# Kernel tuning notes

Hardware: AMD Instinct MI355X
Metric: run time of the kernel (lower is better)

Reference implementation:

```python
import jax, jax.numpy as jnp
import numpy as np

SIGMA = 10
POPULATIONS = 2
LR = 0.001


def _normalize(L, prior):
    # clamp then normalize over populations (logsumexp across the population axis)
    O = L.shape[1]
    L = jnp.clip(L, -5.0, 0.0)
    lse = jax.nn.logsumexp(L.reshape(POPULATIONS, -1, O), axis=0)  # (in/P, O)
    L = L - jnp.tile(lse, (POPULATIONS, 1))
    prior = jnp.clip(prior, -5.0, 0.0)
    prior = prior - jax.nn.logsumexp(prior)
    return L, prior


def _forward(x, L, prior):
    B, T, IN = x.shape
    O = L.shape[1]
    L, prior = _normalize(L, prior)  # matches normalize_probs() in __init__

    # membrane potential: OR of spikes over trailing window of SIGMA steps
    xb = x.astype(bool)
    pot = xb
    for s in range(1, SIGMA):  # fixed small loop (sigma=10)
        pot = pot | jnp.pad(xb, ((0, 0), (s, 0), (0, 0)))[:, :T, :]

    tpre0 = jnp.full((B, IN), -T, dtype=jnp.int32)
    tpost0 = jnp.full((B, O), jnp.iinfo(jnp.int32).max, dtype=jnp.int32)
    base_key = jax.random.key(42)

    pot_T = jnp.transpose(pot, (1, 0, 2))  # (T,B,IN)
    x_T = jnp.transpose(xb, (1, 0, 2))

    def step(carry, inp):
        L, prior, tpre, tpost, t = carry
        pot_t, x_t = inp
        potf = pot_t.astype(L.dtype)
        logits = potf @ L + prior  # (B,O), logits <= 0 so exp is safe
        # torch: softmax(exp(logits)).multinomial == categorical with logits=exp(logits)
        key = jax.random.fold_in(base_key, t)
        widx = jax.random.categorical(key, jnp.exp(logits), axis=-1)  # (B,)
        win = jax.nn.one_hot(widx, O, dtype=L.dtype)
        # trace updates happen BEFORE STDP, as in the torch code
        tpre = jnp.where(x_t, 0, tpre - 1)
        tpost = jnp.where(win > 0, 0, tpost - 1)
        ltp = (tpre >= -SIGMA).astype(L.dtype)
        ltd = (tpre < -SIGMA).astype(L.dtype)
        post = (tpost < 0).astype(L.dtype)
        m_ltp = jnp.einsum('bi,bo->io', ltp, win) / B
        m_ltd = jnp.einsum('bi,bo->io', ltd, win) / B
        m_pp = jnp.einsum('bi,bo->io', potf, post) / B
        decay = (t + 1).astype(L.dtype)  # lr_decay_inverse starts at 1
        # dw = (5 e^{-L} - 1) * LTP.mean - LTD.mean - pre_post.mean ; LTD was negated
        dw = (5.0 * jnp.exp(-L) - 1.0) * m_ltp + m_ltd - m_pp
        L2 = L + (LR / decay) * dw
        wm = jnp.mean(win, axis=0)
        db = (-5.0 * prior - 1.0) * wm - (1.0 - wm)
        p2 = prior + (LR / decay) * db
        L2, p2 = _normalize(L2, p2)
        return (L2, p2, tpre, tpost, t + 1), None

    (Lf, pf, _, _, _), _ = jax.lax.scan(
        step, (L, prior, tpre0, tpost0, jnp.int32(0)), (pot_T, x_T))
    return jnp.concatenate([Lf.reshape(-1), pf])


def setup_inputs() -> dict:
    key = jax.random.key(0)
    k1, k2, k3 = jax.random.split(key, 3)
    B, T, IN, O = 256, 200, 1568, 100
    x = jax.random.randint(k1, (B, T, IN), 0, 2, dtype=jnp.int32)
    log_likelihood = jax.random.uniform(k2, (IN, O), dtype=jnp.float32) * -1.0 - 1.0
    log_prior = jax.random.uniform(k3, (O,), dtype=jnp.float32) * -1.0 - 1.0
    return {"x": x, "log_likelihood": log_likelihood, "log_prior": log_prior}


def reference(x, log_likelihood, log_prior):
    return _forward(x, log_likelihood, log_prior)
```

## Files before the change

kernel.cpp:

```cpp
#include <hip/hip_runtime.h>
#include <stdint.h>

#define BB 256
#define TT 200
#define INN 1568
#define OO 100
#define PAIRS 784
#define NHALF 12800

typedef unsigned long long u64;
typedef __attribute__((ext_vector_type(4))) int v4i;

typedef const __attribute__((address_space(1))) uint32_t* gas_p;
typedef __attribute__((address_space(3))) uint32_t* las_p;
#define GLD16(g, l) __builtin_amdgcn_global_load_lds((gas_p)(g), (las_p)(l), 16, 0, 0)

__device__ __forceinline__ void tf_round(uint32_t& x0, uint32_t& x1, int r) {
    x0 += x1;
    x1 = (x1 << r) | (x1 >> (32 - r));
    x1 ^= x0;
}

__device__ __forceinline__ void threefry(uint32_t k0, uint32_t k1,
                                         uint32_t x0, uint32_t x1,
                                         uint32_t& o0, uint32_t& o1) {
    uint32_t k2 = k0 ^ k1 ^ 0x1BD11BDAu;
    x0 += k0; x1 += k1;
    tf_round(x0,x1,13); tf_round(x0,x1,15); tf_round(x0,x1,26); tf_round(x0,x1,6);
    x0 += k1; x1 += k2 + 1u;
    tf_round(x0,x1,17); tf_round(x0,x1,29); tf_round(x0,x1,16); tf_round(x0,x1,24);
    x0 += k2; x1 += k0 + 2u;
    tf_round(x0,x1,13); tf_round(x0,x1,15); tf_round(x0,x1,26); tf_round(x0,x1,6);
    x0 += k0; x1 += k1 + 3u;
    tf_round(x0,x1,17); tf_round(x0,x1,29); tf_round(x0,x1,16); tf_round(x0,x1,24);
    x0 += k1; x1 += k2 + 4u;
    tf_round(x0,x1,13); tf_round(x0,x1,15); tf_round(x0,x1,26); tf_round(x0,x1,6);
    o0 = x0 + k2; o1 = x1 + k0 + 5u;
}

__global__ __launch_bounds__(256) void k_winbit(const int* __restrict__ x,
                                                uint8_t* __restrict__ widx,
                                                u64* __restrict__ bitB) {
    int tid = threadIdx.x;
    if (blockIdx.x < 200) {
        int idx = blockIdx.x * 256 + tid;
        int t = idx >> 8, b = idx & 255;
        uint32_t fk0, fk1;
        threefry(0u, 42u, 0u, (uint32_t)t, fk0, fk1);
        uint32_t bestkey = 0u;
        int bo = 0;
        int nbase = b * OO;
        for (int o = 0; o < OO; ++o) {
            uint32_t n = (uint32_t)(nbase + o);
            uint32_t lo = (n < NHALF) ? n : n - NHALF;
            uint32_t v0, v1;
            threefry(fk0, fk1, lo, lo + NHALF, v0, v1);
            uint32_t bits = (n < NHALF) ? v0 : v1;
            uint32_t key = bits >> 9;
            if (key > bestkey) { bestkey = key; bo = o; }
        }
        widx[idx] = (uint8_t)bo;
        return;
    }
    int pb = blockIdx.x - 200;
    int wb = pb / 100;
    int t0 = (pb - wb * 100) * 2;
    const v4i* xp = (const v4i*)x;
    u64 acc[4][4];
    #pragma unroll
    for (int q = 0; q < 4; ++q)
        #pragma unroll
        for (int c = 0; c < 4; ++c) acc[q][c] = 0;
    bool x4 = (tid < 16);
    for (int bl = 0; bl < 64; ++bl) {
        size_t base = ((size_t)((wb * 64 + bl) * TT + t0)) * 392;
        u64 bit = 1ull << bl;
        #pragma unroll
        for (int q = 0; q < 3; ++q) {
            v4i v = __builtin_nontemporal_load(&xp[base + tid + q * 256]);
            if (v.x) acc[q][0] |= bit;
            if (v.y) acc[q][1] |= bit;
            if (v.z) acc[q][2] |= bit;
            if (v.w) acc[q][3] |= bit;
        }
        if (x4) {
            v4i v = __builtin_nontemporal_load(&xp[base + tid + 768]);
            if (v.x) acc[3][0] |= bit;
            if (v.y) acc[3][1] |= bit;
            if (v.z) acc[3][2] |= bit;
            if (v.w) acc[3][3] |= bit;
        }
    }
    #pragma unroll
    for (int q = 0; q < 4; ++q) {
        if (q == 3 && !x4) continue;
        int p = tid + q * 256;
        int tp = (p >= 392) ? 1 : 0;
        int iq = p - tp * 392;
        u64* dst = bitB + ((size_t)((t0 + tp) * 4 + wb)) * INN + iq * 4;
        dst[0] = acc[q][0]; dst[1] = acc[q][1];
        dst[2] = acc[q][2]; dst[3] = acc[q][3];
    }
}

__global__ __launch_bounds__(256) void k_fwpost(const uint8_t* __restrict__ widx,
                                                u64* __restrict__ winbits,
                                                u64* __restrict__ postbits,
                                                uint32_t* __restrict__ cnt) {
    __shared__ uint32_t wl32[TT * 65];
    __shared__ int fwl[BB];
    int o = blockIdx.x;
    int tid = threadIdx.x;
    const uint32_t* wsrc = (const uint32_t*)widx;
    for (int g = tid; g < TT * 64; g += 256) {
        int t = g >> 6, w = g & 63;
        wl32[t * 65 + w] = wsrc[g];
    }
    __syncthreads();
    if (tid < 64) {
        int f0 = 255, f1 = 255, f2 = 255, f3 = 255;
        for (int t = 0; t < TT; ++t) {
            uint32_t w4 = wl32[t * 65 + tid];
            if (((w4      ) & 255u) == (uint32_t)o && f0 == 255) f0 = t;
            if (((w4 >>  8) & 255u) == (uint32_t)o && f1 == 255) f1 = t;
            if (((w4 >> 16) & 255u) == (uint32_t)o && f2 == 255) f2 = t;
            if (((w4 >> 24) & 255u) == (uint32_t)o && f3 == 255) f3 = t;
        }
        fwl[4 * tid + 0] = f0; fwl[4 * tid + 1] = f1;
        fwl[4 * tid + 2] = f2; fwl[4 * tid + 3] = f3;
    }
    __syncthreads();
    if (tid < TT) {
        int t = tid;
        u64 wbA[4], pbA[4];
        uint32_t c = 0;
        #pragma unroll
        for (int k = 0; k < 4; ++k) {
            u64 wacc = 0, pacc = 0;
            for (int q2 = 0; q2 < 16; ++q2) {
                uint32_t w4 = wl32[t * 65 + k * 16 + q2];
                #pragma unroll
                for (int j = 0; j < 4; ++j) {
                    int bl = q2 * 4 + j;
                    bool win = (((w4 >> (8 * j)) & 255u) == (uint32_t)o);
                    c += win ? 1u : 0u;
                    bool post = (fwl[k * 64 + q2 * 4 + j] < t) && !win;
                    u64 bit = 1ull << bl;
                    if (win)  wacc |= bit;
                    if (post) pacc |= bit;
                }
            }
            wbA[k] = wacc; pbA[k] = pacc;
        }
        size_t base = (size_t)(t * OO + o) * 4;
        #pragma unroll
        for (int k = 0; k < 4; ++k) {
            winbits[base + k] = wbA[k];
            postbits[base + k] = pbA[k];
        }
        cnt[t * OO + o] = c;
    }
}

#define PBLK 16
#define OBLK 20
#define FTHR 320
#define ROWSTRIDE (4 * INN)
#define PFD 6
#define RS 16

__global__ __launch_bounds__(FTHR) void k_fused(
        const float* __restrict__ L0,
        const float* __restrict__ p0arr,
        const u64* __restrict__ bitB,
        const u64* __restrict__ winbits,
        const u64* __restrict__ postbits,
        const uint32_t* __restrict__ cnt,
        float* __restrict__ outL,
        float* __restrict__ outp) {
    if (blockIdx.x == 49) {
        if (blockIdx.y != 0) return;
        int l = threadIdx.x;
        if (l >= 64) return;
        bool has2 = (l + 64) < OO;
        float pa = p0arr[l];
        float pb = has2 ? p0arr[l + 64] : -1e30f;
        auto normalize = [&]() {
            pa = fminf(fmaxf(pa, -5.0f), 0.0f);
            if (has2) pb = fminf(fmaxf(pb, -5.0f), 0.0f);
            float mx = has2 ? fmaxf(pa, pb) : pa;
            #pragma unroll
            for (int s = 32; s > 0; s >>= 1) mx = fmaxf(mx, __shfl_xor(mx, s, 64));
            float sm = expf(pa - mx) + (has2 ? expf(pb - mx) : 0.0f);
            #pragma unroll
            for (int s = 32; s > 0; s >>= 1) sm += __shfl_xor(sm, s, 64);
            float lse = logf(sm) + mx;
            pa -= lse;
            if (has2) pb -= lse;
        };
        normalize();
        for (int t = 0; t < TT; ++t) {
            float eta = 0.001f / (float)(t + 1);
            float wma = (float)cnt[t * OO + l] * (1.0f / 256.0f);
            pa += eta * ((-5.0f * pa - 1.0f) * wma - (1.0f - wma));
            if (has2) {
                float wmb = (float)cnt[t * OO + l + 64] * (1.0f / 256.0f);
                pb += eta * ((-5.0f * pb - 1.0f) * wmb - (1.0f - wmb));
            }
            normalize();
        }
        outp[l] = pa;
        if (has2) outp[l + 64] = pb;
        return;
    }

    __shared__ __align__(16) u64 rowRing[RS][128];
    __shared__ __align__(16) u64 winRing[RS][80];
    __shared__ __align__(16) u64 postRing[RS][80];
    __shared__ __align__(16) uint32_t cntRing[RS][20];
    __shared__ __align__(16) u64 potL[2][16][10];
    __shared__ __align__(16) u64 ltpL[2][16][10];

    int tid = threadIdx.x;
    int wave = tid >> 6;
    int lane = tid & 63;
    int p0 = blockIdx.x * PBLK;
    int o0 = blockIdx.y * OBLK;

    int pl = tid & 15;
    int ol = tid >> 4;
    int o  = o0 + ol;
    int i0 = p0 + pl;
    int i1 = i0 + PAIRS;

    int lk  = lane >> 3;
    int lpq = (lane & 7) * 2;
    const u64* rowsrc = bitB + (size_t)((lk & 3) * INN + (lk >> 2) * PAIRS + p0 + lpq);

    int wpl = tid & 15;
    int wk  = tid >> 4;
    int eidx = wk * 16 + wpl;

    auto issue = [&](int s) {
        int rr = (s < TT) ? s : (TT - 1);
        int slot = s & (RS - 1);
        if (wave == 0) {
            GLD16(rowsrc + (size_t)rr * ROWSTRIDE, &rowRing[slot][2 * lane]);
        } else if (wave == 1) {
            if (lane < 40)
                GLD16(winbits + ((size_t)rr * OO + o0) * 4 + 2 * lane,
                      &winRing[slot][2 * lane]);
        } else if (wave == 2) {
            if (lane < 40)
                GLD16(postbits + ((size_t)rr * OO + o0) * 4 + 2 * lane,
                      &postRing[slot][2 * lane]);
        } else if (wave == 3) {
            if (lane < 5)
                GLD16(cnt + ((size_t)rr * OO + o0) + 4 * lane,
                      &cntRing[slot][4 * lane]);
        }
    };

    for (int s = 0; s < PFD; ++s) issue(s);
    if (wave < 4) asm volatile("s_waitcnt vmcnt(0)" ::: "memory");
    __builtin_amdgcn_s_barrier();
    if (tid < 128) {
        u64 r0 = rowRing[0][eidx];
        potL[0][wpl][wk] = r0;
        ltpL[0][wpl][wk] = r0;
    }
    float a  = L0[(size_t)i0 * OO + o];
    float b2 = L0[(size_t)i1 * OO + o];
    a  = fminf(fmaxf(a,  -5.0f), 0.0f);
    b2 = fminf(fmaxf(b2, -5.0f), 0.0f);
    {
        float m = fmaxf(a, b2), mn = fminf(a, b2);
        float lse = __logf(1.0f + __expf(mn - m)) + m;
        a -= lse; b2 -= lse;
    }
    asm volatile("s_waitcnt lgkmcnt(0)" ::: "memory");
    __builtin_amdgcn_s_barrier();

    for (int t = 0; t < TT; ++t) {
        int cur = t & 1, nxt = cur ^ 1;
        issue(t + PFD);
        int st = t & (RS - 1);
        u64 W0 = winRing[st][ol * 4 + 0], W1 = winRing[st][ol * 4 + 1];
        u64 W2 = winRing[st][ol * 4 + 2], W3 = winRing[st][ol * 4 + 3];
        u64 S0 = postRing[st][ol * 4 + 0], S1 = postRing[st][ol * 4 + 1];
        u64 S2 = postRing[st][ol * 4 + 2], S3 = postRing[st][ol * 4 + 3];
        const u64* Pp = potL[cur][pl];
        const u64* Lp = ltpL[cur][pl];
        uint32_t lt0 = __popcll(Lp[0] & W0) + __popcll(Lp[1] & W1)
                     + __popcll(Lp[2] & W2) + __popcll(Lp[3] & W3);
        uint32_t lt1 = __popcll(Lp[4] & W0) + __popcll(Lp[5] & W1)
                     + __popcll(Lp[6] & W2) + __popcll(Lp[7] & W3);
        uint32_t pp0 = __popcll(Pp[0] & S0) + __popcll(Pp[1] & S1)
                     + __popcll(Pp[2] & S2) + __popcll(Pp[3] & S3);
        uint32_t pp1 = __popcll(Pp[4] & S0) + __popcll(Pp[5] & S1)
                     + __popcll(Pp[6] & S2) + __popcll(Pp[7] & S3);
        float cwin = (float)cntRing[st][ol];
        float lt0f = (float)lt0, lt1f = (float)lt1;
        float pp0f = (float)pp0, pp1f = (float)pp1;
        float eta = 0.001f / (float)(t + 1);
        float dw0 = (5.0f * __expf(-a)  - 1.0f) * (lt0f * (1.0f/256.0f))
                  + (cwin - lt0f - pp0f) * (1.0f/256.0f);
        float dw1 = (5.0f * __expf(-b2) - 1.0f) * (lt1f * (1.0f/256.0f))
                  + (cwin - lt1f - pp1f) * (1.0f/256.0f);
        a  += eta * dw0;
        b2 += eta * dw1;
        a  = fminf(fmaxf(a,  -5.0f), 0.0f);
        b2 = fminf(fmaxf(b2, -5.0f), 0.0f);
        float m = fmaxf(a, b2), mn = fminf(a, b2);
        float lse = __logf(1.0f + __expf(mn - m)) + m;
        a -= lse; b2 -= lse;
        if (tid < 128) {
            int rbase = t + 1 - 10;
            u64 acc = 0;
            #pragma unroll
            for (int j = 1; j <= 10; ++j) {
                int rr = rbase + j; if (rr < 0) rr = 0;
                acc |= rowRing[rr & (RS - 1)][eidx];
            }
            int rz = (rbase < 0) ? 0 : rbase;
            u64 lt = acc | rowRing[rz & (RS - 1)][eidx];
            potL[nxt][wpl][wk] = acc;
            ltpL[nxt][wpl][wk] = lt;
        }
        if (wave < 4) {
            asm volatile("s_waitcnt vmcnt(4) lgkmcnt(0)" ::: "memory");
        } else {
            asm volatile("s_waitcnt lgkmcnt(0)" ::: "memory");
        }
        __builtin_amdgcn_s_barrier();
    }
    outL[(size_t)i0 * OO + o] = a;
    outL[(size_t)i1 * OO + o] = b2;
}

extern "C" void kernel_launch(void* const* d_in, const int* in_sizes, int n_in,
                              void* d_out, int out_size, void* d_ws, size_t ws_size,
                              hipStream_t stream) {
    const int*   x  = (const int*)d_in[0];
    const float* L0 = (const float*)d_in[1];
    const float* p0 = (const float*)d_in[2];
    float* out = (float*)d_out;

    char* ws = (char*)d_ws;
    size_t off = 0;
    auto alloc = [&](size_t bytes) -> void* {
        off = (off + 255) & ~(size_t)255;
        void* p = ws + off;
        off += bytes;
        return p;
    };
    uint8_t*  widx     = (uint8_t*) alloc((size_t)TT * BB);
    uint32_t* cnt      = (uint32_t*)alloc((size_t)TT * OO * 4);
    u64*      winbits  = (u64*)     alloc((size_t)TT * OO * 4 * 8);
    u64*      postbits = (u64*)     alloc((size_t)TT * OO * 4 * 8);
    u64*      bitB     = (u64*)     alloc((size_t)TT * 4 * INN * 8);
    (void)ws_size;

    hipLaunchKernelGGL(k_winbit, dim3(600), dim3(256), 0, stream, x, widx, bitB);
    hipLaunchKernelGGL(k_fwpost, dim3(OO), dim3(256), 0, stream,
                       widx, winbits, postbits, cnt);
    hipLaunchKernelGGL(k_fused, dim3(50, 5), dim3(FTHR), 0, stream,
                       L0, p0, bitB, winbits, postbits, cnt,
                       out, out + (size_t)INN * OO);
}
```

Measured before the change: 611.6 us.

## Merge three kernels into one persistent kernel with software grid barriers

```diff
diff --git a/kernel.cpp b/kernel.cpp
--- a/kernel.cpp
+++ b/kernel.cpp
@@ -7,6 +7,9 @@
 #define OO 100
 #define PAIRS 784
 #define NHALF 12800
+#define NBLK 240
+#define UNITS 686
+#define ROWSTRIDE (4 * INN)
 
 typedef unsigned long long u64;
 typedef __attribute__((ext_vector_type(4))) int v4i;
@@ -38,12 +41,47 @@
     o0 = x0 + k2; o1 = x1 + k0 + 5u;
 }
 
-__global__ __launch_bounds__(256) void k_winbit(const int* __restrict__ x,
-                                                uint8_t* __restrict__ widx,
-                                                u64* __restrict__ bitB) {
-    int tid = threadIdx.x;
-    if (blockIdx.x < 200) {
-        int idx = blockIdx.x * 256 + tid;
+struct FusedSM {
+    u64 rows[8][16][64];
+    u64 wp[8][8][128];
+    u64 potC[8][2][8][10];
+    u64 ltpC[8][2][8][10];
+    uint32_t cntR[8][8][16];
+};
+struct FwSM { uint32_t wl32[TT * 65]; int fwl[BB]; };
+union SMem { FusedSM f; FwSM w; uint32_t claim; };
+
+__device__ __forceinline__ void gridsync(uint32_t* c) {
+    __syncthreads();
+    if (threadIdx.x == 0) {
+        __threadfence();
+        __hip_atomic_fetch_add(c, 1u, __ATOMIC_ACQ_REL, __HIP_MEMORY_SCOPE_AGENT);
+        while (__hip_atomic_load(c, __ATOMIC_ACQUIRE, __HIP_MEMORY_SCOPE_AGENT)
+               < (uint32_t)NBLK)
+            __builtin_amdgcn_s_sleep(8);
+        __threadfence();
+    }
+    __syncthreads();
+}
+
+__global__ __launch_bounds__(512) void k_mono(
+        const int* __restrict__ x,
+        const float* __restrict__ L0,
+        const float* __restrict__ p0arr,
+        uint32_t* __restrict__ syncc,
+        uint8_t* __restrict__ widx,
+        uint32_t* __restrict__ cntg,
+        u64* __restrict__ winbits,
+        u64* __restrict__ postbits,
+        u64* __restrict__ bitB,
+        float* __restrict__ outL,
+        float* __restrict__ outp) {
+    __shared__ SMem sm;
+    const int tid = threadIdx.x;
+    const int bid = blockIdx.x;
+
+    if (bid < 100) {
+        int idx = bid * 512 + tid;
         int t = idx >> 8, b = idx & 255;
         uint32_t fk0, fk1;
         threefry(0u, 42u, 0u, (uint32_t)t, fk0, fk1);
@@ -60,282 +98,303 @@
             if (key > bestkey) { bestkey = key; bo = o; }
         }
         widx[idx] = (uint8_t)bo;
-        return;
     }
-    int pb = blockIdx.x - 200;
-    int wb = pb / 100;
-    int t0 = (pb - wb * 100) * 2;
-    const v4i* xp = (const v4i*)x;
-    u64 acc[4][4];
-    #pragma unroll
-    for (int q = 0; q < 4; ++q)
-        #pragma unroll
-        for (int c = 0; c < 4; ++c) acc[q][c] = 0;
-    bool x4 = (tid < 16);
-    for (int bl = 0; bl < 64; ++bl) {
-        size_t base = ((size_t)((wb * 64 + bl) * TT + t0)) * 392;
-        u64 bit = 1ull << bl;
-        #pragma unroll
-        for (int q = 0; q < 3; ++q) {
-            v4i v = __builtin_nontemporal_load(&xp[base + tid + q * 256]);
-            if (v.x) acc[q][0] |= bit;
-            if (v.y) acc[q][1] |= bit;
-            if (v.z) acc[q][2] |= bit;
-            if (v.w) acc[q][3] |= bit;
-        }
-        if (x4) {
-            v4i v = __builtin_nontemporal_load(&xp[base + tid + 768]);
-            if (v.x) acc[3][0] |= bit;
-            if (v.y) acc[3][1] |= bit;
-            if (v.z) acc[3][2] |= bit;
-            if (v.w) acc[3][3] |= bit;
-        }
+    gridsync(&syncc[0]);
+
+    if (bid < 100) {
+        const uint32_t* wsrc = (const uint32_t*)widx;
+        for (int g = tid; g < TT * 64; g += 512)
+            sm.w.wl32[(g >> 6) * 65 + (g & 63)] = wsrc[g];
+        __syncthreads();
+        int o = bid;
+        if (tid < 64) {
+            int f0 = 255, f1 = 255, f2 = 255, f3 = 255;
+            for (int t = 0; t < TT; ++t) {
+                uint32_t w4 = sm.w.wl32[t * 65 + tid];
+                if (((w4      ) & 255u) == (uint32_t)o && f0 == 255) f0 = t;
+                if (((w4 >>  8) & 255u) == (uint32_t)o && f1 == 255) f1 = t;
+                if (((w4 >> 16) & 255u) == (uint32_t)o && f2 == 255) f2 = t;
+                if (((w4 >> 24) & 255u) == (uint32_t)o && f3 == 255) f3 = t;
+            }
+            sm.w.fwl[4 * tid + 0] = f0; sm.w.fwl[4 * tid + 1] = f1;
+            sm.w.fwl[4 * tid + 2] = f2; sm.w.fwl[4 * tid + 3] = f3;
+        }
+        __syncthreads();
+        if (tid < TT) {
+            int t = tid;
+            u64 wbA[4], pbA[4];
+            uint32_t c = 0;
+            #pragma unroll
+            for (int k = 0; k < 4; ++k) {
+                u64 wacc = 0, pacc = 0;
+                for (int q2 = 0; q2 < 16; ++q2) {
+                    uint32_t w4 = sm.w.wl32[t * 65 + k * 16 + q2];
+                    #pragma unroll
+                    for (int j = 0; j < 4; ++j) {
+                        int bl = q2 * 4 + j;
+                        bool win = (((w4 >> (8 * j)) & 255u) == (uint32_t)o);
+                        c += win ? 1u : 0u;
+                        bool post = (sm.w.fwl[k * 64 + q2 * 4 + j] < t) && !win;
+                        u64 bit = 1ull << bl;
+                        if (win)  wacc |= bit;
+                        if (post) pacc |= bit;
+                    }
+                }
+                wbA[k] = wacc; pbA[k] = pacc;
+            }
+            size_t base = (size_t)(t * OO + o) * 4;
+            #pragma unroll
+            for (int k = 0; k < 4; ++k) {
+                winbits[base + k] = wbA[k];
+                postbits[base + k] = pbA[k];
+            }
+            cntg[t * OO + o] = c;
+        }
+        __syncthreads();
     }
-    #pragma unroll
-    for (int q = 0; q < 4; ++q) {
-        if (q == 3 && !x4) continue;
-        int p = tid + q * 256;
-        int tp = (p >= 392) ? 1 : 0;
-        int iq = p - tp * 392;
-        u64* dst = bitB + ((size_t)((t0 + tp) * 4 + wb)) * INN + iq * 4;
-        dst[0] = acc[q][0]; dst[1] = acc[q][1];
-        dst[2] = acc[q][2]; dst[3] = acc[q][3];
+
+    {
+        const v4i* xp = (const v4i*)x;
+        for (;;) {
+            __syncthreads();
+            if (tid == 0)
+                sm.claim = __hip_atomic_fetch_add(&syncc[2], 1u, __ATOMIC_RELAXED,
+                                                  __HIP_MEMORY_SCOPE_AGENT);
+            __syncthreads();
+            uint32_t u = sm.claim;
+            if (u >= 200u) break;
+            int wb = u & 3, tc = u >> 2;
+            u64 acc[4][4];
+            #pragma unroll
+            for (int q = 0; q < 4; ++q)
+                #pragma unroll
+                for (int c = 0; c < 4; ++c) acc[q][c] = 0;
+            bool x4 = (tid < 32);
+            for (int bl = 0; bl < 64; ++bl) {
+                size_t base = ((size_t)((wb * 64 + bl) * TT + tc * 4)) * 392;
+                u64 bit = 1ull << bl;
+                #pragma unroll
+                for (int q = 0; q < 3; ++q) {
+                    v4i v = __builtin_nontemporal_load(&xp[base + tid + q * 512]);
+                    if (v.x) acc[q][0] |= bit;
+                    if (v.y) acc[q][1] |= bit;
+                    if (v.z) acc[q][2] |= bit;
+                    if (v.w) acc[q][3] |= bit;
+                }
+                if (x4) {
+                    v4i v = __builtin_nontemporal_load(&xp[base + tid + 1536]);
+                    if (v.x) acc[3][0] |= bit;
+                    if (v.y) acc[3][1] |= bit;
+                    if (v.z) acc[3][2] |= bit;
+                    if (v.w) acc[3][3] |= bit;
+                }
+            }
+            #pragma unroll
+            for (int q = 0; q < 4; ++q) {
+                if (q == 3 && !x4) continue;
+                int p = tid + q * 512;
+                int tp = (p >= 1176) ? 3 : (p >= 784) ? 2 : (p >= 392) ? 1 : 0;
+                int iq = p - tp * 392;
+                u64* dst = bitB + ((size_t)((tc * 4 + tp) * 4 + wb)) * INN + iq * 4;
+                dst[0] = acc[q][0]; dst[1] = acc[q][1];
+                dst[2] = acc[q][2]; dst[3] = acc[q][3];
+            }
+        }
     }
-}
-
-__global__ __launch_bounds__(256) void k_fwpost(const uint8_t* __restrict__ widx,
-                                                u64* __restrict__ winbits,
-                                                u64* __restrict__ postbits,
-                                                uint32_t* __restrict__ cnt) {
-    __shared__ uint32_t wl32[TT * 65];
-    __shared__ int fwl[BB];
-    int o = blockIdx.x;
-    int tid = threadIdx.x;
-    const uint32_t* wsrc = (const uint32_t*)widx;
-    for (int g = tid; g < TT * 64; g += 256) {
-        int t = g >> 6, w = g & 63;
-        wl32[t * 65 + w] = wsrc[g];
+    gridsync(&syncc[1]);
+
+    {
+        const int wv = tid >> 6, lane = tid & 63;
+        int u = bid + NBLK * wv;
+        if (u > UNITS) return;
+        if (u == UNITS) {
+            int l = lane;
+            bool has2 = (l + 64) < OO;
+            float pa = p0arr[l];
+            float pb = has2 ? p0arr[l + 64] : -1e30f;
+            auto norm = [&]() {
+                pa = fminf(fmaxf(pa, -5.0f), 0.0f);
+                if (has2) pb = fminf(fmaxf(pb, -5.0f), 0.0f);
+                float mx = has2 ? fmaxf(pa, pb) : pa;
+                #pragma unroll
+                for (int s = 32; s > 0; s >>= 1) mx = fmaxf(mx, __shfl_xor(mx, s, 64));
+                float smv = expf(pa - mx) + (has2 ? expf(pb - mx) : 0.0f);
+                #pragma unroll
+                for (int s = 32; s > 0; s >>= 1) smv += __shfl_xor(smv, s, 64);
+                float lse = logf(smv) + mx;
+                pa -= lse;
+                if (has2) pb -= lse;
+            };
+            norm();
+            uint32_t na = cntg[l];
+            uint32_t nb = has2 ? cntg[l + 64] : 0u;
+            for (int t = 0; t < TT; ++t) {
+                float ca = (float)na, cb = (float)nb;
+                if (t < TT - 1) {
+                    na = cntg[(t + 1) * OO + l];
+                    nb = has2 ? cntg[(t + 1) * OO + l + 64] : 0u;
+                }
+                float eta = 0.001f / (float)(t + 1);
+                float wma = ca * (1.0f / 256.0f);
+                pa += eta * ((-5.0f * pa - 1.0f) * wma - (1.0f - wma));
+                if (has2) {
+                    float wmb = cb * (1.0f / 256.0f);
+                    pb += eta * ((-5.0f * pb - 1.0f) * wmb - (1.0f - wmb));
+                }
+                norm();
+            }
+            outp[l] = pa;
+            if (has2) outp[l + 64] = pb;
+            return;
+        }
+
+        const int pg = u % 98, og = u / 98;
+        const int p0 = pg * 8, o0 = og * 16;
+        const int pl = lane & 7, ol = lane >> 3;
+        const int oA = o0 + ol, oB = oA + 8;
+        const int i0 = p0 + pl, i1 = i0 + PAIRS;
+        const bool actA = (oA < OO), actB = (oB < OO);
+
+        const int e0 = (lane & 31) * 2;
+        const int wk0 = e0 >> 3, wpl0 = e0 & 7;
+        const u64* rowg = bitB + (size_t)((wk0 & 3) * INN + (wk0 >> 2) * PAIRS
+                                          + p0 + wpl0);
+        const int lw = lane & 31;
+        const u64* wpg = (lane < 32) ? winbits : postbits;
+        const bool wpact = (o0 + (lw >> 1)) < OO;
+        const bool cntact = (lane < 8) && ((o0 + (lane & 3) * 4) < OO);
+
+        auto issueG = [&](int G) {
+            int r0 = 2 * G;
+            {
+                int rr = r0 + (lane >> 5); if (rr > TT - 1) rr = TT - 1;
+                GLD16(rowg + (size_t)rr * ROWSTRIDE,
+                      (las_p)&sm.f.rows[wv][r0 & 15][0]);
+            }
+            {
+                int rr = r0; if (rr > TT - 1) rr = TT - 1;
+                if (wpact)
+                    GLD16(wpg + ((size_t)rr * OO + o0) * 4 + 2 * lw,
+                          (las_p)&sm.f.wp[wv][r0 & 7][0]);
+            }
+            {
+                int rr = r0 + 1; if (rr > TT - 1) rr = TT - 1;
+                if (wpact)
+                    GLD16(wpg + ((size_t)rr * OO + o0) * 4 + 2 * lw,
+                          (las_p)&sm.f.wp[wv][(r0 + 1) & 7][0]);
+            }
+            {
+                if (cntact) {
+                    int rr = r0 + (lane >> 2); if (rr > TT - 1) rr = TT - 1;
+                    GLD16(cntg + (size_t)rr * OO + o0 + (lane & 3) * 4,
+                          (las_p)&sm.f.cntR[wv][r0 & 7][0]);
+                }
+            }
+        };
+
+        float aA = actA ? L0[(size_t)i0 * OO + oA] : -1.0f;
+        float bA = actA ? L0[(size_t)i1 * OO + oA] : -1.0f;
+        float aB = actB ? L0[(size_t)i0 * OO + oB] : -1.0f;
+        float bB = actB ? L0[(size_t)i1 * OO + oB] : -1.0f;
+        {
+            aA = fminf(fmaxf(aA, -5.0f), 0.0f);
+            bA = fminf(fmaxf(bA, -5.0f), 0.0f);
+            float m = fmaxf(aA, bA), mn = fminf(aA, bA);
+            float lse = __logf(1.0f + __expf(mn - m)) + m;
+            aA -= lse; bA -= lse;
+            aB = fminf(fmaxf(aB, -5.0f), 0.0f);
+            bB = fminf(fmaxf(bB, -5.0f), 0.0f);
+            float m2 = fmaxf(aB, bB), mn2 = fminf(aB, bB);
+            float lse2 = __logf(1.0f + __expf(mn2 - m2)) + m2;
+            aB -= lse2; bB -= lse2;
+        }
+
+        auto chainstep = [&](int t, int sp) {
+            int s = t & 7;
+            const u64* wpS = &sm.f.wp[wv][s][0];
+            const u64* P = sm.f.potC[wv][sp][pl];
+            const u64* Lt = sm.f.ltpC[wv][sp][pl];
+            u64 P0 = P[0], P1 = P[1], P2 = P[2], P3 = P[3];
+            u64 P4 = P[4], P5 = P[5], P6 = P[6], P7 = P[7];
+            u64 Q0 = Lt[0], Q1 = Lt[1], Q2 = Lt[2], Q3 = Lt[3];
+            u64 Q4 = Lt[4], Q5 = Lt[5], Q6 = Lt[6], Q7 = Lt[7];
+            float eta = 0.001f / (float)(t + 1);
+            {
+                u64 W0 = wpS[ol*4+0], W1 = wpS[ol*4+1], W2 = wpS[ol*4+2], W3 = wpS[ol*4+3];
+                u64 S0 = wpS[64+ol*4+0], S1 = wpS[64+ol*4+1], S2 = wpS[64+ol*4+2], S3 = wpS[64+ol*4+3];
+                float cw = (float)sm.f.cntR[wv][s][ol];
+                float lt0 = (float)(__popcll(Q0&W0)+__popcll(Q1&W1)+__popcll(Q2&W2)+__popcll(Q3&W3));
+                float lt1 = (float)(__popcll(Q4&W0)+__popcll(Q5&W1)+__popcll(Q6&W2)+__popcll(Q7&W3));
+                float pp0 = (float)(__popcll(P0&S0)+__popcll(P1&S1)+__popcll(P2&S2)+__popcll(P3&S3));
+                float pp1 = (float)(__popcll(P4&S0)+__popcll(P5&S1)+__popcll(P6&S2)+__popcll(P7&S3));
+                float dw0 = (5.0f*__expf(-aA) - 1.0f)*(lt0*(1.0f/256.0f))
+                          + (cw - lt0 - pp0)*(1.0f/256.0f);
+                float dw1 = (5.0f*__expf(-bA) - 1.0f)*(lt1*(1.0f/256.0f))
+                          + (cw - lt1 - pp1)*(1.0f/256.0f);
+                aA += eta*dw0; bA += eta*dw1;
+                aA = fminf(fmaxf(aA,-5.0f),0.0f);
+                bA = fminf(fmaxf(bA,-5.0f),0.0f);
+                float m = fmaxf(aA,bA), mn = fminf(aA,bA);
+                float lse = __logf(1.0f + __expf(mn-m)) + m;
+                aA -= lse; bA -= lse;
+            }
+            {
+                u64 W0 = wpS[(ol+8)*4+0], W1 = wpS[(ol+8)*4+1], W2 = wpS[(ol+8)*4+2], W3 = wpS[(ol+8)*4+3];
+                u64 S0 = wpS[64+(ol+8)*4+0], S1 = wpS[64+(ol+8)*4+1], S2 = wpS[64+(ol+8)*4+2], S3 = wpS[64+(ol+8)*4+3];
+                float cw = (float)sm.f.cntR[wv][s][ol+8];
+                float lt0 = (float)(__popcll(Q0&W0)+__popcll(Q1&W1)+__popcll(Q2&W2)+__popcll(Q3&W3));
+                float lt1 = (float)(__popcll(Q4&W0)+__popcll(Q5&W1)+__popcll(Q6&W2)+__popcll(Q7&W3));
+                float pp0 = (float)(__popcll(P0&S0)+__popcll(P1&S1)+__popcll(P2&S2)+__popcll(P3&S3));
+                float pp1 = (float)(__popcll(P4&S0)+__popcll(P5&S1)+__popcll(P6&S2)+__popcll(P7&S3));
+                float dw0 = (5.0f*__expf(-aB) - 1.0f)*(lt0*(1.0f/256.0f))
+                          + (cw - lt0 - pp0)*(1.0f/256.0f);
+                float dw1 = (5.0f*__expf(-bB) - 1.0f)*(lt1*(1.0f/256.0f))
+                          + (cw - lt1 - pp1)*(1.0f/256.0f);
+                aB += eta*dw0; bB += eta*dw1;
+                aB = fminf(fmaxf(aB,-5.0f),0.0f);
+                bB = fminf(fmaxf(bB,-5.0f),0.0f);
+                float m = fmaxf(aB,bB), mn = fminf(aB,bB);
+                float lse = __logf(1.0f + __expf(mn-m)) + m;
+                aB -= lse; bB -= lse;
+            }
+        };
+
+        issueG(0);
+        issueG(1);
+        for (int I = 0; I < 100; ++I) {
+            issueG(I + 2);
+            asm volatile("s_waitcnt vmcnt(8)" ::: "memory");
+            int b0 = 2 * I;
+            u64 com = 0;
+            #pragma unroll
+            for (int j = 8; j >= 0; --j) {
+                int r = b0 - j; r = (r < 0) ? 0 : r;
+                com |= sm.f.rows[wv][r & 15][lane];
+            }
+            int r9 = b0 - 9;   r9 = (r9 < 0) ? 0 : r9;
+            int r10 = b0 - 10; r10 = (r10 < 0) ? 0 : r10;
+            u64 v9  = sm.f.rows[wv][r9 & 15][lane];
+            u64 v10 = sm.f.rows[wv][r10 & 15][lane];
+            u64 vt2 = sm.f.rows[wv][(b0 + 1) & 15][lane];
+            u64 pot1 = com | v9;
+            u64 pot2 = com | vt2;
+            sm.f.potC[wv][0][lane & 7][lane >> 3] = pot1;
+            sm.f.potC[wv][1][lane & 7][lane >> 3] = pot2;
+            sm.f.ltpC[wv][0][lane & 7][lane >> 3] = pot1 | v10;
+            sm.f.ltpC[wv][1][lane & 7][lane >> 3] = pot2 | v9;
+            asm volatile("s_waitcnt lgkmcnt(0)" ::: "memory");
+            chainstep(b0, 0);
+            chainstep(b0 + 1, 1);
+        }
+        if (actA) {
+            outL[(size_t)i0 * OO + oA] = aA;
+            outL[(size_t)i1 * OO + oA] = bA;
+        }
+        if (actB) {
+            outL[(size_t)i0 * OO + oB] = aB;
+            outL[(size_t)i1 * OO + oB] = bB;
+        }
     }
-    __syncthreads();
-    if (tid < 64) {
-        int f0 = 255, f1 = 255, f2 = 255, f3 = 255;
-        for (int t = 0; t < TT; ++t) {
-            uint32_t w4 = wl32[t * 65 + tid];
-            if (((w4      ) & 255u) == (uint32_t)o && f0 == 255) f0 = t;
-            if (((w4 >>  8) & 255u) == (uint32_t)o && f1 == 255) f1 = t;
-            if (((w4 >> 16) & 255u) == (uint32_t)o && f2 == 255) f2 = t;
-            if (((w4 >> 24) & 255u) == (uint32_t)o && f3 == 255) f3 = t;
-        }
-        fwl[4 * tid + 0] = f0; fwl[4 * tid + 1] = f1;
-        fwl[4 * tid + 2] = f2; fwl[4 * tid + 3] = f3;
-    }
-    __syncthreads();
-    if (tid < TT) {
-        int t = tid;
-        u64 wbA[4], pbA[4];
-        uint32_t c = 0;
-        #pragma unroll
-        for (int k = 0; k < 4; ++k) {
-            u64 wacc = 0, pacc = 0;
-            for (int q2 = 0; q2 < 16; ++q2) {
-                uint32_t w4 = wl32[t * 65 + k * 16 + q2];
-                #pragma unroll
-                for (int j = 0; j < 4; ++j) {
-                    int bl = q2 * 4 + j;
-                    bool win = (((w4 >> (8 * j)) & 255u) == (uint32_t)o);
-                    c += win ? 1u : 0u;
-                    bool post = (fwl[k * 64 + q2 * 4 + j] < t) && !win;
-                    u64 bit = 1ull << bl;
-                    if (win)  wacc |= bit;
-                    if (post) pacc |= bit;
-                }
-            }
-            wbA[k] = wacc; pbA[k] = pacc;
-        }
-        size_t base = (size_t)(t * OO + o) * 4;
-        #pragma unroll
-        for (int k = 0; k < 4; ++k) {
-            winbits[base + k] = wbA[k];
-            postbits[base + k] = pbA[k];
-        }
-        cnt[t * OO + o] = c;
-    }
-}
-
-#define PBLK 16
-#define OBLK 20
-#define FTHR 320
-#define ROWSTRIDE (4 * INN)
-#define PFD 6
-#define RS 16
-
-__global__ __launch_bounds__(FTHR) void k_fused(
-        const float* __restrict__ L0,
-        const float* __restrict__ p0arr,
-        const u64* __restrict__ bitB,
-        const u64* __restrict__ winbits,
-        const u64* __restrict__ postbits,
-        const uint32_t* __restrict__ cnt,
-        float* __restrict__ outL,
-        float* __restrict__ outp) {
-    if (blockIdx.x == 49) {
-        if (blockIdx.y != 0) return;
-        int l = threadIdx.x;
-        if (l >= 64) return;
-        bool has2 = (l + 64) < OO;
-        float pa = p0arr[l];
-        float pb = has2 ? p0arr[l + 64] : -1e30f;
-        auto normalize = [&]() {
-            pa = fminf(fmaxf(pa, -5.0f), 0.0f);
-            if (has2) pb = fminf(fmaxf(pb, -5.0f), 0.0f);
-            float mx = has2 ? fmaxf(pa, pb) : pa;
-            #pragma unroll
-            for (int s = 32; s > 0; s >>= 1) mx = fmaxf(mx, __shfl_xor(mx, s, 64));
-            float sm = expf(pa - mx) + (has2 ? expf(pb - mx) : 0.0f);
-            #pragma unroll
-            for (int s = 32; s > 0; s >>= 1) sm += __shfl_xor(sm, s, 64);
-            float lse = logf(sm) + mx;
-            pa -= lse;
-            if (has2) pb -= lse;
-        };
-        normalize();
-        for (int t = 0; t < TT; ++t) {
-            float eta = 0.001f / (float)(t + 1);
-            float wma = (float)cnt[t * OO + l] * (1.0f / 256.0f);
-            pa += eta * ((-5.0f * pa - 1.0f) * wma - (1.0f - wma));
-            if (has2) {
-                float wmb = (float)cnt[t * OO + l + 64] * (1.0f / 256.0f);
-                pb += eta * ((-5.0f * pb - 1.0f) * wmb - (1.0f - wmb));
-            }
-            normalize();
-        }
-        outp[l] = pa;
-        if (has2) outp[l + 64] = pb;
-        return;
-    }
-
-    __shared__ __align__(16) u64 rowRing[RS][128];
-    __shared__ __align__(16) u64 winRing[RS][80];
-    __shared__ __align__(16) u64 postRing[RS][80];
-    __shared__ __align__(16) uint32_t cntRing[RS][20];
-    __shared__ __align__(16) u64 potL[2][16][10];
-    __shared__ __align__(16) u64 ltpL[2][16][10];
-
-    int tid = threadIdx.x;
-    int wave = tid >> 6;
-    int lane = tid & 63;
-    int p0 = blockIdx.x * PBLK;
-    int o0 = blockIdx.y * OBLK;
-
-    int pl = tid & 15;
-    int ol = tid >> 4;
-    int o  = o0 + ol;
-    int i0 = p0 + pl;
-    int i1 = i0 + PAIRS;
-
-    int lk  = lane >> 3;
-    int lpq = (lane & 7) * 2;
-    const u64* rowsrc = bitB + (size_t)((lk & 3) * INN + (lk >> 2) * PAIRS + p0 + lpq);
-
-    int wpl = tid & 15;
-    int wk  = tid >> 4;
-    int eidx = wk * 16 + wpl;
-
-    auto issue = [&](int s) {
-        int rr = (s < TT) ? s : (TT - 1);
-        int slot = s & (RS - 1);
-        if (wave == 0) {
-            GLD16(rowsrc + (size_t)rr * ROWSTRIDE, &rowRing[slot][2 * lane]);
-        } else if (wave == 1) {
-            if (lane < 40)
-                GLD16(winbits + ((size_t)rr * OO + o0) * 4 + 2 * lane,
-                      &winRing[slot][2 * lane]);
-        } else if (wave == 2) {
-            if (lane < 40)
-                GLD16(postbits + ((size_t)rr * OO + o0) * 4 + 2 * lane,
-                      &postRing[slot][2 * lane]);
-        } else if (wave == 3) {
-            if (lane < 5)
-                GLD16(cnt + ((size_t)rr * OO + o0) + 4 * lane,
-                      &cntRing[slot][4 * lane]);
-        }
-    };
-
-    for (int s = 0; s < PFD; ++s) issue(s);
-    if (wave < 4) asm volatile("s_waitcnt vmcnt(0)" ::: "memory");
-    __builtin_amdgcn_s_barrier();
-    if (tid < 128) {
-        u64 r0 = rowRing[0][eidx];
-        potL[0][wpl][wk] = r0;
-        ltpL[0][wpl][wk] = r0;
-    }
-    float a  = L0[(size_t)i0 * OO + o];
-    float b2 = L0[(size_t)i1 * OO + o];
-    a  = fminf(fmaxf(a,  -5.0f), 0.0f);
-    b2 = fminf(fmaxf(b2, -5.0f), 0.0f);
-    {
-        float m = fmaxf(a, b2), mn = fminf(a, b2);
-        float lse = __logf(1.0f + __expf(mn - m)) + m;
-        a -= lse; b2 -= lse;
-    }
-    asm volatile("s_waitcnt lgkmcnt(0)" ::: "memory");
-    __builtin_amdgcn_s_barrier();
-
-    for (int t = 0; t < TT; ++t) {
-        int cur = t & 1, nxt = cur ^ 1;
-        issue(t + PFD);
-        int st = t & (RS - 1);
-        u64 W0 = winRing[st][ol * 4 + 0], W1 = winRing[st][ol * 4 + 1];
-        u64 W2 = winRing[st][ol * 4 + 2], W3 = winRing[st][ol * 4 + 3];
-        u64 S0 = postRing[st][ol * 4 + 0], S1 = postRing[st][ol * 4 + 1];
-        u64 S2 = postRing[st][ol * 4 + 2], S3 = postRing[st][ol * 4 + 3];
-        const u64* Pp = potL[cur][pl];
-        const u64* Lp = ltpL[cur][pl];
-        uint32_t lt0 = __popcll(Lp[0] & W0) + __popcll(Lp[1] & W1)
-                     + __popcll(Lp[2] & W2) + __popcll(Lp[3] & W3);
-        uint32_t lt1 = __popcll(Lp[4] & W0) + __popcll(Lp[5] & W1)
-                     + __popcll(Lp[6] & W2) + __popcll(Lp[7] & W3);
-        uint32_t pp0 = __popcll(Pp[0] & S0) + __popcll(Pp[1] & S1)
-                     + __popcll(Pp[2] & S2) + __popcll(Pp[3] & S3);
-        uint32_t pp1 = __popcll(Pp[4] & S0) + __popcll(Pp[5] & S1)
-                     + __popcll(Pp[6] & S2) + __popcll(Pp[7] & S3);
-        float cwin = (float)cntRing[st][ol];
-        float lt0f = (float)lt0, lt1f = (float)lt1;
-        float pp0f = (float)pp0, pp1f = (float)pp1;
-        float eta = 0.001f / (float)(t + 1);
-        float dw0 = (5.0f * __expf(-a)  - 1.0f) * (lt0f * (1.0f/256.0f))
-                  + (cwin - lt0f - pp0f) * (1.0f/256.0f);
-        float dw1 = (5.0f * __expf(-b2) - 1.0f) * (lt1f * (1.0f/256.0f))
-                  + (cwin - lt1f - pp1f) * (1.0f/256.0f);
-        a  += eta * dw0;
-        b2 += eta * dw1;
-        a  = fminf(fmaxf(a,  -5.0f), 0.0f);
-        b2 = fminf(fmaxf(b2, -5.0f), 0.0f);
-        float m = fmaxf(a, b2), mn = fminf(a, b2);
-        float lse = __logf(1.0f + __expf(mn - m)) + m;
-        a -= lse; b2 -= lse;
-        if (tid < 128) {
-            int rbase = t + 1 - 10;
-            u64 acc = 0;
-            #pragma unroll
-            for (int j = 1; j <= 10; ++j) {
-                int rr = rbase + j; if (rr < 0) rr = 0;
-                acc |= rowRing[rr & (RS - 1)][eidx];
-            }
-            int rz = (rbase < 0) ? 0 : rbase;
-            u64 lt = acc | rowRing[rz & (RS - 1)][eidx];
-            potL[nxt][wpl][wk] = acc;
-            ltpL[nxt][wpl][wk] = lt;
-        }
-        if (wave < 4) {
-            asm volatile("s_waitcnt vmcnt(4) lgkmcnt(0)" ::: "memory");
-        } else {
-            asm volatile("s_waitcnt lgkmcnt(0)" ::: "memory");
-        }
-        __builtin_amdgcn_s_barrier();
-    }
-    outL[(size_t)i0 * OO + o] = a;
-    outL[(size_t)i1 * OO + o] = b2;
 }
 
 extern "C" void kernel_launch(void* const* d_in, const int* in_sizes, int n_in,
@@ -354,17 +413,16 @@
         off += bytes;
         return p;
     };
+    uint32_t* syncc    = (uint32_t*)alloc(256);
     uint8_t*  widx     = (uint8_t*) alloc((size_t)TT * BB);
-    uint32_t* cnt      = (uint32_t*)alloc((size_t)TT * OO * 4);
+    uint32_t* cntg     = (uint32_t*)alloc((size_t)TT * OO * 4);
     u64*      winbits  = (u64*)     alloc((size_t)TT * OO * 4 * 8);
     u64*      postbits = (u64*)     alloc((size_t)TT * OO * 4 * 8);
     u64*      bitB     = (u64*)     alloc((size_t)TT * 4 * INN * 8);
     (void)ws_size;
 
-    hipLaunchKernelGGL(k_winbit, dim3(600), dim3(256), 0, stream, x, widx, bitB);
-    hipLaunchKernelGGL(k_fwpost, dim3(OO), dim3(256), 0, stream,
-                       widx, winbits, postbits, cnt);
-    hipLaunchKernelGGL(k_fused, dim3(50, 5), dim3(FTHR), 0, stream,
-                       L0, p0, bitB, winbits, postbits, cnt,
+    hipMemsetAsync(syncc, 0, 256, stream);
+    hipLaunchKernelGGL(k_mono, dim3(NBLK), dim3(512), 0, stream,
+                       x, L0, p0, syncc, widx, cntg, winbits, postbits, bitB,
                        out, out + (size_t)INN * OO);
 }
```

After: 699.7 us. 14.4% more time.
